# Optimization experiments

Hardware: AMD Instinct MI355X
Metric: run time of the kernel (lower is better)

The kernel has to match this reference:

```python
import jax, jax.numpy as jnp
import numpy as np

# Conv2dfft forward (no spectral compression: preserve_energy=None, index_back=None, out_size=None)
# Implements cross-correlation (DL convolution) via rfft2 / irfft2, matching the torch module's
# padding and output-size logic:
#   out_H = H - HH + 1 + 2*pad ; init_fft = H + 2*pad + max(out_H, HH) - 1

PAD = 1  # padding from init_kwargs


def setup_inputs() -> dict:
    key = jax.random.key(0)
    k1, k2, k3 = jax.random.split(key, 3)
    x = jax.random.normal(k1, (32, 128, 32, 32), dtype=jnp.float32)
    w = jax.random.normal(k2, (128, 128, 3, 3), dtype=jnp.float32) * 0.1
    b = jax.random.normal(k3, (128,), dtype=jnp.float32)
    return {"x": x, "w": w, "b": b}


def reference(x, w, b):
    N, C, H, W = x.shape
    F, _, HH, WW = w.shape
    out_H = H - HH + 1 + 2 * PAD
    out_W = W - WW + 1 + 2 * PAD
    init_fft_H = H + 2 * PAD + max(out_H, HH) - 1  # 65
    init_fft_W = W + 2 * PAD + max(out_W, WW) - 1  # 65

    # pad input: explicit conv padding + zero-pad up to FFT grid
    fft_pad_H = init_fft_H - 2 * PAD - H
    fft_pad_W = init_fft_W - 2 * PAD - W
    px = jnp.pad(x, ((0, 0), (0, 0), (PAD, PAD + fft_pad_H), (PAD, PAD + fft_pad_W)))
    pw = jnp.pad(w, ((0, 0), (0, 0), (0, init_fft_H - HH), (0, init_fft_W - WW)))

    xfft = jnp.fft.rfft2(px)                     # [N,C,65,33] complex64
    yfft = jnp.fft.rfft2(pw)                     # [F,C,65,33] complex64

    # cross-correlation: multiply by conj(filter fft), accumulate over input channels
    prod = jnp.einsum('nchw,fchw->nfhw', xfft, jnp.conj(yfft))
    full = jnp.fft.irfft2(prod, s=(init_fft_H, init_fft_W))  # [N,F,65,65]
    out = full[:, :, :out_H, :out_W] + b[None, :, None, None]
    return out
```

## Files before the change

kernel.cpp:

```cpp
#include <hip/hip_runtime.h>


typedef __attribute__((ext_vector_type(8))) short bf16x8;
typedef __attribute__((ext_vector_type(4))) float f32x4;

#define N_IMG 32
#define C_IN  128
#define F_OUT 128
#define HW    32
#define HPAD  34

__device__ __forceinline__ unsigned short f2bf(float f) {
    union { float f; unsigned u; } v; v.f = f;
    unsigned r = v.u + 0x7fffu + ((v.u >> 16) & 1u);
    return (unsigned short)(r >> 16);
}

__global__ __launch_bounds__(256) void pack_w_kernel(const float* __restrict__ w,
                                                     unsigned short* __restrict__ wpk) {
    int idx = blockIdx.x * 256 + threadIdx.x;
    int c8  = idx & 7;
    int f   = (idx >> 3) & 127;
    int qk  = (idx >> 10) & 3;
    int u   = idx >> 12;
    int cc  = u / 9;
    int tap = u - cc * 9;
    wpk[idx] = f2bf(w[(f * C_IN + cc * 32 + qk * 8 + c8) * 9 + tap]);
}

__global__ __launch_bounds__(256, 1) void conv_gemm_kernel(
    const float* __restrict__ x,
    const unsigned short* __restrict__ wpk,
    const float* __restrict__ bias,
    float* __restrict__ out)
{
    __shared__ alignas(16) unsigned short lds_x[204 * C_IN];
    __shared__ alignas(16) unsigned short lds_w[3][3 * 4096];

    const int tid  = threadIdx.x;
    const int lane = tid & 63;
    const int wave = tid >> 6;
    const int qk   = lane >> 4;
    const int l15  = lane & 15;

    const int band = blockIdx.x & 7;
    const int n    = blockIdx.x >> 3;
    const int fh   = wave >> 1;
    const int rp   = wave & 1;
    const int f0   = fh * 64;

    if (tid < 192) {
        int dh = tid / 32, rem = tid & 31;
        int wp = (rem & 1) * 33, qc = rem >> 1;
        int rr = dh * 34 + wp;
        *(bf16x8*)&lds_x[rr * C_IN + ((qc ^ (rr & 15)) << 3)] =
            (bf16x8){0, 0, 0, 0, 0, 0, 0, 0};
    }
    {
        const int w_    = lane & 31;
        const int chalf = lane >> 5;
        for (int dh = 0; dh < 6; ++dh) {
            const int h = band * 4 - 1 + dh;
            const bool valid = (h >= 0) && (h < HW);
            #pragma unroll
            for (int g2 = 0; g2 < 2; ++g2) {
                const int c0 = (wave * 2 + g2) * 16 + chalf * 8;
                bf16x8 v;
                if (valid) {
                    #pragma unroll
                    for (int k = 0; k < 8; ++k) {
                        float f = x[((n * C_IN + (c0 + k)) * HW + h) * HW + w_];
                        v[k] = (short)f2bf(f);
                    }
                } else {
                    #pragma unroll
                    for (int k = 0; k < 8; ++k) v[k] = 0;
                }
                const int rr = dh * 34 + (w_ + 1);
                const int qc = c0 >> 3;
                *(bf16x8*)&lds_x[rr * C_IN + ((qc ^ (rr & 15)) << 3)] = v;
            }
        }
    }
    __builtin_amdgcn_sched_barrier(0);

    #define STAGE_W3(ccv, t0v, bufv) do {                                       \
        const unsigned short* wsrc = wpk + ((ccv) * 9 + (t0v)) * 4096;          \
        _Pragma("unroll")                                                       \
        for (int j_ = 0; j_ < 6; ++j_) {                                        \
            int p_ = tid + j_ * 256;                                            \
            __builtin_amdgcn_global_load_lds(                                   \
                (const __attribute__((address_space(1))) void*)(wsrc + p_ * 8), \
                (__attribute__((address_space(3))) void*)(&lds_w[bufv][p_ * 8]),\
                16, 0, 0);                                                      \
        }                                                                       \
    } while (0)

    STAGE_W3(0, 0, 0);
    STAGE_W3(0, 3, 1);
    __builtin_amdgcn_sched_barrier(0);

    f32x4 acc[4][4];
    #pragma unroll
    for (int mi = 0; mi < 4; ++mi)
        #pragma unroll
        for (int ni = 0; ni < 4; ++ni)
            acc[mi][ni] = (f32x4){0.f, 0.f, 0.f, 0.f};

    int rrb[4];
    #pragma unroll
    for (int ni = 0; ni < 4; ++ni)
        rrb[ni] = (rp * 2 + (ni >> 1)) * HPAD + (ni & 1) * 16 + l15;

    const int af_base = qk * 1024 + (f0 + l15) * 8;

    asm volatile("s_waitcnt vmcnt(6) lgkmcnt(0)" ::: "memory");
    __builtin_amdgcn_s_barrier();
    __builtin_amdgcn_sched_barrier(0);

    #define COMPUTE3(bufv, ccv, T0)                                             \
        _Pragma("unroll")                                                       \
        for (int tl = 0; tl < 3; ++tl) {                                        \
            const int tap = (T0) + tl;                                          \
            const int r = tap / 3, s = tap - 3 * (tap / 3);                     \
            bf16x8 af[4], bf[4];                                                \
            _Pragma("unroll")                                                   \
            for (int mi = 0; mi < 4; ++mi)                                      \
                af[mi] = *(const bf16x8*)&lds_w[bufv][tl * 4096 + af_base + mi * 128]; \
            _Pragma("unroll")                                                   \
            for (int ni = 0; ni < 4; ++ni) {                                    \
                int rr = rrb[ni] + r * HPAD + s;                                \
                int ph = ((ccv) * 4 + qk) ^ (rr & 15);                          \
                bf[ni] = *(const bf16x8*)&lds_x[rr * C_IN + ph * 8];            \
            }                                                                   \
            _Pragma("unroll")                                                   \
            for (int mi = 0; mi < 4; ++mi)                                      \
                _Pragma("unroll")                                               \
                for (int ni = 0; ni < 4; ++ni)                                  \
                    acc[mi][ni] = __builtin_amdgcn_mfma_f32_16x16x32_bf16(      \
                        af[mi], bf[ni], acc[mi][ni], 0, 0, 0);                  \
        }

    #define PHASE_FULL(cc2, t02, b2, bcur, ccv, t0v) do {                       \
        STAGE_W3(cc2, t02, b2);                                                 \
        COMPUTE3(bcur, ccv, t0v);                                               \
        asm volatile("s_waitcnt vmcnt(6)" ::: "memory");                        \
        __builtin_amdgcn_s_barrier();                                           \
        __builtin_amdgcn_sched_barrier(0);                                      \
    } while (0)

    PHASE_FULL(0, 6, 2, 0, 0, 0);
    PHASE_FULL(1, 0, 0, 1, 0, 3);
    PHASE_FULL(1, 3, 1, 2, 0, 6);
    PHASE_FULL(1, 6, 2, 0, 1, 0);
    PHASE_FULL(2, 0, 0, 1, 1, 3);
    PHASE_FULL(2, 3, 1, 2, 1, 6);
    PHASE_FULL(2, 6, 2, 0, 2, 0);
    PHASE_FULL(3, 0, 0, 1, 2, 3);
    PHASE_FULL(3, 3, 1, 2, 2, 6);
    PHASE_FULL(3, 6, 2, 0, 3, 0);
    COMPUTE3(1, 3, 3);
    asm volatile("s_waitcnt vmcnt(0)" ::: "memory");
    __builtin_amdgcn_s_barrier();
    __builtin_amdgcn_sched_barrier(0);
    COMPUTE3(2, 3, 6);

    const int h0 = band * 4 + rp * 2;
    #pragma unroll
    for (int mi = 0; mi < 4; ++mi) {
        const int f_base = f0 + mi * 16 + qk * 4;
        float bv[4];
        #pragma unroll
        for (int r2 = 0; r2 < 4; ++r2) bv[r2] = bias[f_base + r2];
        #pragma unroll
        for (int ni = 0; ni < 4; ++ni) {
            const int h  = h0 + (ni >> 1);
            const int w2 = (ni & 1) * 16 + l15;
            #pragma unroll
            for (int r2 = 0; r2 < 4; ++r2) {
                out[((unsigned)(n * F_OUT + f_base + r2) * HW + h) * HW + w2] =
                    acc[mi][ni][r2] + bv[r2];
            }
        }
    }
    #undef STAGE_W3
    #undef COMPUTE3
    #undef PHASE_FULL
}

extern "C" void kernel_launch(void* const* d_in, const int* in_sizes, int n_in,
                              void* d_out, int out_size, void* d_ws, size_t ws_size,
                              hipStream_t stream) {
    const float* x = (const float*)d_in[0];
    const float* w = (const float*)d_in[1];
    const float* b = (const float*)d_in[2];
    float* out = (float*)d_out;

    unsigned short* wpk = (unsigned short*)d_ws;

    pack_w_kernel<<<576, 256, 0, stream>>>(w, wpk);
    conv_gemm_kernel<<<N_IMG * 8, 256, 0, stream>>>(x, wpk, b, out);
}
```

Measured before the change: 83.76 us.

## Stream input channel chunks into LDS while computing earlier chunks

The prologue now loads only the first 32-channel chunk of the input band into LDS. The remaining three chunks are fetched into registers during the weight-staged compute phases and written to LDS after each phase's MFMA work. This hides the large up-front global load of the input behind tensor-core compute. In exchange it adds register pressure and an lgkmcnt wait per phase, and it depends on the chunk-to-phase ordering being correct (chunk k must be written before the compute that uses it).

```diff
diff --git a/kernel.cpp b/kernel.cpp
--- a/kernel.cpp
+++ b/kernel.cpp
@@ -42,6 +42,8 @@
     const int wave = tid >> 6;
     const int qk   = lane >> 4;
     const int l15  = lane & 15;
+    const int w_    = lane & 31;
+    const int chalf = lane >> 5;
 
     const int band = blockIdx.x & 7;
     const int n    = blockIdx.x >> 3;
@@ -56,31 +58,25 @@
         *(bf16x8*)&lds_x[rr * C_IN + ((qc ^ (rr & 15)) << 3)] =
             (bf16x8){0, 0, 0, 0, 0, 0, 0, 0};
     }
-    {
-        const int w_    = lane & 31;
-        const int chalf = lane >> 5;
-        for (int dh = 0; dh < 6; ++dh) {
-            const int h = band * 4 - 1 + dh;
-            const bool valid = (h >= 0) && (h < HW);
+    #pragma unroll
+    for (int sl = 0; sl < 3; ++sl) {
+        const int slot = wave * 3 + sl;
+        const int dh = slot >> 1, g2 = slot & 1;
+        const int h = band * 4 - 1 + dh;
+        const bool valid = (h >= 0) && (h < HW);
+        const int c0 = g2 * 16 + chalf * 8;
+        bf16x8 v;
+        if (valid) {
             #pragma unroll
-            for (int g2 = 0; g2 < 2; ++g2) {
-                const int c0 = (wave * 2 + g2) * 16 + chalf * 8;
-                bf16x8 v;
-                if (valid) {
-                    #pragma unroll
-                    for (int k = 0; k < 8; ++k) {
-                        float f = x[((n * C_IN + (c0 + k)) * HW + h) * HW + w_];
-                        v[k] = (short)f2bf(f);
-                    }
-                } else {
-                    #pragma unroll
-                    for (int k = 0; k < 8; ++k) v[k] = 0;
-                }
-                const int rr = dh * 34 + (w_ + 1);
-                const int qc = c0 >> 3;
-                *(bf16x8*)&lds_x[rr * C_IN + ((qc ^ (rr & 15)) << 3)] = v;
-            }
+            for (int k = 0; k < 8; ++k)
+                v[k] = (short)f2bf(x[((n * C_IN + (c0 + k)) * HW + h) * HW + w_]);
+        } else {
+            #pragma unroll
+            for (int k = 0; k < 8; ++k) v[k] = 0;
         }
+        const int rr = dh * 34 + (w_ + 1);
+        const int qc = c0 >> 3;
+        *(bf16x8*)&lds_x[rr * C_IN + ((qc ^ (rr & 15)) << 3)] = v;
     }
     __builtin_amdgcn_sched_barrier(0);
 
@@ -149,15 +145,49 @@
         __builtin_amdgcn_sched_barrier(0);                                      \
     } while (0)
 
-    PHASE_FULL(0, 6, 2, 0, 0, 0);
-    PHASE_FULL(1, 0, 0, 1, 0, 3);
-    PHASE_FULL(1, 3, 1, 2, 0, 6);
-    PHASE_FULL(1, 6, 2, 0, 1, 0);
-    PHASE_FULL(2, 0, 0, 1, 1, 3);
-    PHASE_FULL(2, 3, 1, 2, 1, 6);
-    PHASE_FULL(2, 6, 2, 0, 2, 0);
-    PHASE_FULL(3, 0, 0, 1, 2, 3);
-    PHASE_FULL(3, 3, 1, 2, 2, 6);
+    #define PHASE_XW(cc2, t02, b2, bcur, ccv, t0v, xcc, kk) do {                \
+        const int slot_ = (kk) * 4 + wave;                                      \
+        const int dh_ = slot_ >> 1, g2_ = slot_ & 1;                            \
+        const int h_ = band * 4 - 1 + dh_;                                      \
+        const bool valid_ = (h_ >= 0) && (h_ < HW);                             \
+        const int c0_ = (xcc) * 32 + g2_ * 16 + chalf * 8;                      \
+        float xf_[8];                                                           \
+        if (valid_) {                                                           \
+            _Pragma("unroll")                                                   \
+            for (int k2 = 0; k2 < 8; ++k2)                                      \
+                xf_[k2] = x[((n * C_IN + (c0_ + k2)) * HW + h_) * HW + w_];     \
+        }                                                                       \
+        __builtin_amdgcn_sched_barrier(0);                                      \
+        STAGE_W3(cc2, t02, b2);                                                 \
+        COMPUTE3(bcur, ccv, t0v);                                               \
+        __builtin_amdgcn_sched_barrier(0);                                      \
+        {                                                                       \
+            bf16x8 xv_;                                                         \
+            if (valid_) {                                                       \
+                _Pragma("unroll")                                               \
+                for (int k2 = 0; k2 < 8; ++k2) xv_[k2] = (short)f2bf(xf_[k2]);  \
+            } else {                                                            \
+                _Pragma("unroll")                                               \
+                for (int k2 = 0; k2 < 8; ++k2) xv_[k2] = 0;                     \
+            }                                                                   \
+            const int rr_ = dh_ * 34 + (w_ + 1);                                \
+            const int qc_ = c0_ >> 3;                                           \
+            *(bf16x8*)&lds_x[rr_ * C_IN + ((qc_ ^ (rr_ & 15)) << 3)] = xv_;     \
+        }                                                                       \
+        asm volatile("s_waitcnt vmcnt(6) lgkmcnt(0)" ::: "memory");             \
+        __builtin_amdgcn_s_barrier();                                           \
+        __builtin_amdgcn_sched_barrier(0);                                      \
+    } while (0)
+
+    PHASE_XW(0, 6, 2, 0, 0, 0, 1, 0);
+    PHASE_XW(1, 0, 0, 1, 0, 3, 1, 1);
+    PHASE_XW(1, 3, 1, 2, 0, 6, 1, 2);
+    PHASE_XW(1, 6, 2, 0, 1, 0, 2, 0);
+    PHASE_XW(2, 0, 0, 1, 1, 3, 2, 1);
+    PHASE_XW(2, 3, 1, 2, 1, 6, 2, 2);
+    PHASE_XW(2, 6, 2, 0, 2, 0, 3, 0);
+    PHASE_XW(3, 0, 0, 1, 2, 3, 3, 1);
+    PHASE_XW(3, 3, 1, 2, 2, 6, 3, 2);
     PHASE_FULL(3, 6, 2, 0, 3, 0);
     COMPUTE3(1, 3, 3);
     asm volatile("s_waitcnt vmcnt(0)" ::: "memory");
@@ -186,6 +216,7 @@
     #undef STAGE_W3
     #undef COMPUTE3
     #undef PHASE_FULL
+    #undef PHASE_XW
 }
 
 extern "C" void kernel_launch(void* const* d_in, const int* in_sizes, int n_in,
```

Result: slower. 86.53 us (+3.3%).
